# Kernel optimization log

Hardware: AMD Instinct MI355X
Metric: run time of the kernel (lower is better)

Reference implementation:

```python
import jax, jax.numpy as jnp
import numpy as np

E = 8          # num experts
TOPK = 2
D = 1024       # emb_size (expert hidden == emb_size)


def setup_inputs() -> dict:
    key = jax.random.key(0)
    ks = jax.random.split(key, 8)
    s = 1.0 / np.sqrt(D)
    x = jax.random.normal(ks[0], (4, 1024, D), dtype=jnp.float32)
    gate_W = jax.random.uniform(ks[1], (E, D), jnp.float32, -s, s)   # torch Linear weight (out,in)
    gate_b = jax.random.uniform(ks[2], (E,), jnp.float32, -s, s)
    w1 = jax.random.uniform(ks[3], (E, D, D), jnp.float32, -s, s)    # per-expert first Linear (out,in)
    b1 = jax.random.uniform(ks[4], (E, D), jnp.float32, -s, s)
    w2 = jax.random.uniform(ks[5], (E, D, D), jnp.float32, -s, s)    # per-expert second Linear (out,in)
    b2 = jax.random.uniform(ks[6], (E, D), jnp.float32, -s, s)
    return {"x": x, "gate_W": gate_W, "gate_b": gate_b,
            "w1": w1, "b1": b1, "w2": w2, "b2": b2}


def reference(x, gate_W, gate_b, w1, b1, w2, b2):
    x_shape = x.shape
    xt = x.reshape(-1, x_shape[-1])                       # [N, D]

    # gating
    gate_logits = xt @ gate_W.T + gate_b                  # [N, E]
    gate_prob = jax.nn.softmax(gate_logits, axis=-1)      # [N, E]
    top_w, top_i = jax.lax.top_k(gate_prob, TOPK)         # [N, K]
    top_w = jax.nn.softmax(top_w, axis=-1)                # renormalize over top-k

    # dense per-expert MLP: h = relu(x @ W1^T + b1); o = h @ W2^T + b2
    h = jax.nn.relu(jnp.einsum('nd,ehd->neh', xt, w1) + b1[None])   # [N, E, D]
    o = jnp.einsum('neh,eoh->neo', h, w2) + b2[None]                # [N, E, D]

    # gather top-k expert outputs per token and combine with weights
    o_top = jnp.take_along_axis(o, top_i[:, :, None], axis=1)       # [N, K, D]
    y = jnp.sum(o_top * top_w[:, :, None], axis=1)                  # [N, D]

    return y.reshape(x_shape), gate_prob
```

## Files before the change

kernel.cpp:

```cpp
#include <hip/hip_runtime.h>

#define NTOK 4096
#define DIM 1024
#define NE 8
#define NPAIR (NTOK * 2)

typedef __bf16 bf16x8 __attribute__((ext_vector_type(8)));
typedef float floatx4 __attribute__((ext_vector_type(4)));

__device__ __forceinline__ unsigned short f2bf(float f) {
  unsigned u = __float_as_uint(f);
  u = u + 0x7fffu + ((u >> 16) & 1u);
  return (unsigned short)(u >> 16);
}
__device__ __forceinline__ float bf2f(unsigned short h) {
  return __uint_as_float(((unsigned)h) << 16);
}

__device__ __forceinline__ void gld_lds16(const unsigned short* g, unsigned short* l) {
  __builtin_amdgcn_global_load_lds(
      (const __attribute__((address_space(1))) void*)g,
      (__attribute__((address_space(3))) void*)l, 16, 0, 0);
}

__global__ __launch_bounds__(256) void gate_kernel(
    const float* __restrict__ x, const float* __restrict__ gW,
    const float* __restrict__ gb,
    float* __restrict__ gp_out, int2* __restrict__ tops,
    float* __restrict__ pairw, int* __restrict__ cnt, int* __restrict__ done)
{
  const int tid = threadIdx.x;
  if (blockIdx.x == 0) {
    if (tid < NE) cnt[tid] = 0;
    if (tid == NE) *done = 0;
  }
  const int lane = tid & 63;
  const int wid = tid >> 6;
  const int t = blockIdx.x * 4 + wid;

  float4 xv[4];
#pragma unroll
  for (int j = 0; j < 4; j++)
    xv[j] = ((const float4*)(x + (size_t)t * DIM))[lane + 64 * j];

  float p[NE];
#pragma unroll
  for (int e = 0; e < NE; e++) {
    const float4* gwe = (const float4*)(gW + e * DIM);
    float s = 0.f;
#pragma unroll
    for (int j = 0; j < 4; j++) {
      float4 g = gwe[lane + 64 * j];
      s += xv[j].x * g.x + xv[j].y * g.y + xv[j].z * g.z + xv[j].w * g.w;
    }
    p[e] = s;
  }
#pragma unroll
  for (int e = 0; e < NE; e++) {
#pragma unroll
    for (int off = 32; off >= 1; off >>= 1) p[e] += __shfl_xor(p[e], off);
  }

  float m = -1e30f;
#pragma unroll
  for (int e = 0; e < NE; e++) { p[e] += gb[e]; m = fmaxf(m, p[e]); }
  float s = 0.f;
  float pr[NE];
#pragma unroll
  for (int e = 0; e < NE; e++) { pr[e] = __expf(p[e] - m); s += pr[e]; }
  float inv = 1.f / s;
#pragma unroll
  for (int e = 0; e < NE; e++) pr[e] *= inv;

  if (lane < NE) gp_out[(size_t)t * NE + lane] = pr[lane];

  if (lane == 0) {
    int i0 = 0;
#pragma unroll
    for (int e = 1; e < NE; e++) if (pr[e] > pr[i0]) i0 = e;
    int i1 = (i0 == 0) ? 1 : 0;
#pragma unroll
    for (int e = 0; e < NE; e++) if (e != i0 && pr[e] > pr[i1]) i1 = e;
    float d = __expf(pr[i1] - pr[i0]);
    float w0 = 1.f / (1.f + d);
    tops[t] = make_int2(i0, i1);
    pairw[t * 2] = w0;
    pairw[t * 2 + 1] = 1.f - w0;
  }
}

__global__ __launch_bounds__(256) void bin_sched_kernel(
    const int2* __restrict__ tops, int* __restrict__ cnt,
    int* __restrict__ bucket,
    int* __restrict__ posmap,
    int* __restrict__ done, int* __restrict__ base,
    int* __restrict__ sched, int* __restrict__ sched_n)
{
  const int t = blockIdx.x * 256 + threadIdx.x;
  const int lane = threadIdx.x & 63;
  int2 ti = tops[t];
#pragma unroll
  for (int slot = 0; slot < 2; slot++) {
    int e = slot ? ti.y : ti.x;
#pragma unroll
    for (int ex = 0; ex < NE; ex++) {
      bool mine = (e == ex);
      unsigned long long mask = __ballot(mine);
      if (mask) {
        int leader = __ffsll((long long)mask) - 1;
        int total = __popcll(mask);
        int prefix = __popcll(mask & ((1ull << lane) - 1ull));
        int idx = 0;
        if (lane == leader) idx = atomicAdd(&cnt[ex], total);
        idx = __shfl(idx, leader) + prefix;
        if (mine) {
          bucket[ex * NTOK + idx] = t * 2 + slot;
          posmap[t * 2 + slot] = (ex << 16) | idx;
        }
      }
    }
  }
  __syncthreads();
  if (threadIdx.x == 0) {
    if (atomicAdd(done, 1) == gridDim.x - 1) {
      int b = 0, pos = 0;
      for (int e = 0; e < NE; e++) {
        int c = atomicAdd(&cnt[e], 0);
        base[e] = b;
        int tiles = (c + 127) >> 7;
        for (int i = 0; i < tiles; i++) {
          int valid = c - i * 128; if (valid > 128) valid = 128;
          sched[pos++] = (e << 20) | (i << 8) | valid;
        }
        b += c;
      }
      base[NE] = b;
      *sched_n = pos;
    }
  }
}

__global__ __launch_bounds__(256) void cvt_kernel(
    const float4* __restrict__ src, ushort4* __restrict__ dst)
{
  const int i = blockIdx.x * 256 + threadIdx.x;
  float4 v = src[i];
  ushort4 o;
  o.x = f2bf(v.x); o.y = f2bf(v.y); o.z = f2bf(v.z); o.w = f2bf(v.w);
  dst[i] = o;
}

__global__ __launch_bounds__(256) void gather_kernel(
    const float* __restrict__ x, const int* __restrict__ bucket,
    const int* __restrict__ base, unsigned short* __restrict__ A_pack)
{
  const int p = blockIdx.x;
  int e = 0;
#pragma unroll
  for (int k = 0; k < NE - 1; k++) if (p >= base[k + 1]) e = k + 1;
  const int pair = bucket[e * NTOK + (p - base[e])];
  const int tok = pair >> 1;
  const int tid = threadIdx.x;
  float4 v = ((const float4*)(x + (size_t)tok * DIM))[tid];
  ushort4 o;
  o.x = f2bf(v.x); o.y = f2bf(v.y); o.z = f2bf(v.z); o.w = f2bf(v.w);
  ((ushort4*)(A_pack + (size_t)p * DIM))[tid] = o;
}

template <int RELU>
__global__ __launch_bounds__(256) void ffn_gemm(
    const unsigned short* __restrict__ A,
    const unsigned short* __restrict__ B,
    const float* __restrict__ bias,
    const int* __restrict__ base,
    const int* __restrict__ sched, const int* __restrict__ sched_n,
    unsigned short* __restrict__ Out)
{
  const int l = blockIdx.x;
  const int xcd = l & 7;
  const int w = l >> 3;
  const int nt = w & 7;
  const int slot = xcd * 9 + (w >> 3);
  if (slot >= *sched_n) return;
  const int se = sched[slot];
  const int e = se >> 20;
  const int mt = (se >> 8) & 0xfff;
  const int valid = se & 255;
  const int arow0 = base[e] + mt * 128;

  __shared__ unsigned short lda[128 * 64];
  __shared__ unsigned short ldb[128 * 64];

  const int tid = threadIdx.x;
  const int lane = tid & 63;
  const int wid = tid >> 6;

  const unsigned short* ap[4];
  const unsigned short* bp[4];
#pragma unroll
  for (int j = 0; j < 4; j++) {
    int g = wid * 4 + j;
    int row = g * 8 + (lane >> 3);
    int gran = (lane & 7) ^ (row & 7);
    int prow = arow0 + row;
    if (prow > NPAIR - 1) prow = NPAIR - 1;
    ap[j] = A + (size_t)prow * DIM + (gran << 3);
    bp[j] = B + ((size_t)e * DIM + nt * 128 + row) * DIM + (gran << 3);
  }

  floatx4 acc[4][4] = {};
  const int wm = (wid & 1) * 64;
  const int wn = (wid >> 1) * 64;
  const int quad = lane >> 4;
  const int cl = lane & 15;
  const int sw = cl & 7;

  for (int k0 = 0; k0 < 16; k0++) {
#pragma unroll
    for (int j = 0; j < 4; j++) {
      int g = wid * 4 + j;
      gld_lds16(ap[j], &lda[g * 512]);
      gld_lds16(bp[j], &ldb[g * 512]);
      ap[j] += 64;
      bp[j] += 64;
    }
    __syncthreads();
#pragma unroll
    for (int kk = 0; kk < 64; kk += 32) {
      const int gb = (kk >> 3) + quad;
      const int goff = ((gb ^ sw) << 3);
      bf16x8 af[4], bfr[4];
#pragma unroll
      for (int mi = 0; mi < 4; mi++)
        af[mi] = *(const bf16x8*)&lda[(wm + mi * 16 + cl) * 64 + goff];
#pragma unroll
      for (int ni = 0; ni < 4; ni++)
        bfr[ni] = *(const bf16x8*)&ldb[(wn + ni * 16 + cl) * 64 + goff];
#pragma unroll
      for (int mi = 0; mi < 4; mi++)
#pragma unroll
        for (int ni = 0; ni < 4; ni++)
          acc[mi][ni] = __builtin_amdgcn_mfma_f32_16x16x32_bf16(af[mi], bfr[ni], acc[mi][ni], 0, 0, 0);
    }
    if (k0 < 15) __syncthreads();
  }

#pragma unroll
  for (int ni = 0; ni < 4; ni++) {
    int col = nt * 128 + wn + ni * 16 + cl;
    float bval = bias[e * DIM + col];
#pragma unroll
    for (int mi = 0; mi < 4; mi++) {
#pragma unroll
      for (int reg = 0; reg < 4; reg++) {
        int rl = wm + mi * 16 + quad * 4 + reg;
        if (rl < valid) {
          float v = acc[mi][ni][reg] + bval;
          if (RELU) v = fmaxf(v, 0.f);
          Out[(size_t)(arow0 + rl) * DIM + col] = f2bf(v);
        }
      }
    }
  }
}

__global__ __launch_bounds__(256) void combine_kernel(
    const unsigned short* __restrict__ o, const int* __restrict__ posmap,
    const int* __restrict__ base, const float* __restrict__ pairw,
    float* __restrict__ y)
{
  const int t = blockIdx.x;
  const int tid = threadIdx.x;
  const int pm0 = posmap[t * 2], pm1 = posmap[t * 2 + 1];
  const int p0 = base[pm0 >> 16] + (pm0 & 0xffff);
  const int p1 = base[pm1 >> 16] + (pm1 & 0xffff);
  const float w0 = pairw[t * 2], w1 = pairw[t * 2 + 1];
  ushort4 a = ((const ushort4*)(o + (size_t)p0 * DIM))[tid];
  ushort4 b = ((const ushort4*)(o + (size_t)p1 * DIM))[tid];
  float4 r;
  r.x = w0 * bf2f(a.x) + w1 * bf2f(b.x);
  r.y = w0 * bf2f(a.y) + w1 * bf2f(b.y);
  r.z = w0 * bf2f(a.z) + w1 * bf2f(b.z);
  r.w = w0 * bf2f(a.w) + w1 * bf2f(b.w);
  ((float4*)(y + (size_t)t * DIM))[tid] = r;
}

extern "C" void kernel_launch(void* const* d_in, const int* in_sizes, int n_in,
                              void* d_out, int out_size, void* d_ws, size_t ws_size,
                              hipStream_t stream) {
  const float* x  = (const float*)d_in[0];
  const float* gW = (const float*)d_in[1];
  const float* gb = (const float*)d_in[2];
  const float* w1 = (const float*)d_in[3];
  const float* b1 = (const float*)d_in[4];
  const float* w2 = (const float*)d_in[5];
  const float* b2 = (const float*)d_in[6];
  float* y  = (float*)d_out;
  float* gp = (float*)d_out + (size_t)NTOK * DIM;

  char* ws = (char*)d_ws;
  unsigned short* A_pack = (unsigned short*)(ws);
  unsigned short* w2_bf  = (unsigned short*)(ws);
  unsigned short* h_pack = (unsigned short*)(ws + (size_t)(16u << 20));
  unsigned short* w1_bf  = (unsigned short*)(ws + (size_t)(32u << 20));
  unsigned short* o_pack = (unsigned short*)(ws + (size_t)(32u << 20));
  char* tail = ws + (size_t)(48u << 20);
  int*   cnt     = (int*)(tail);
  int*   done    = cnt + NE;
  int*   base    = done + 1;
  int*   sched   = base + NE + 1;
  int*   sched_n = sched + 128;
  int*   bucket  = sched_n + 1;
  float* pairw   = (float*)(bucket + NE * NTOK);
  int2*  tops    = (int2*)(pairw + NPAIR);
  int*   posmap  = (int*)(tops + NTOK);

  const int cvt_blocks = (NE * DIM * DIM / 4) / 256;
  gate_kernel<<<NTOK / 4, 256, 0, stream>>>(x, gW, gb, gp, tops, pairw, cnt, done);
  bin_sched_kernel<<<NTOK / 256, 256, 0, stream>>>(tops, cnt, bucket, posmap, done,
                                                   base, sched, sched_n);
  cvt_kernel<<<cvt_blocks, 256, 0, stream>>>((const float4*)w1, (ushort4*)w1_bf);
  gather_kernel<<<NPAIR, 256, 0, stream>>>(x, bucket, base, A_pack);
  ffn_gemm<1><<<576, 256, 0, stream>>>(A_pack, w1_bf, b1, base, sched, sched_n, h_pack);
  cvt_kernel<<<cvt_blocks, 256, 0, stream>>>((const float4*)w2, (ushort4*)w2_bf);
  ffn_gemm<0><<<576, 256, 0, stream>>>(h_pack, w2_bf, b2, base, sched, sched_n, o_pack);
  combine_kernel<<<NTOK, 256, 0, stream>>>(o_pack, posmap, base, pairw, y);
}
```

Measured before the change: 238.7 us.

## Halve GEMM N-tile, fuse w1 conversion into gather, pre-convert x in gate

The expert GEMMs now use a 128x64 output tile instead of 128x128, with twice as many blocks (1152) and a new slot/tile mapping across XCDs, to raise occupancy and wave count. The w1 fp32->bf16 conversion is folded into the gather kernel (cvt_blocks equals NPAIR), removing one launch. The gate kernel also writes a bf16 copy of x, so the gather becomes a plain bf16 copy. Smaller tiles lower per-block reuse of A and add extra A loads in exchange for parallelism.

```diff
diff --git a/kernel.cpp b/kernel.cpp
--- a/kernel.cpp
+++ b/kernel.cpp
@@ -25,7 +25,7 @@
 
 __global__ __launch_bounds__(256) void gate_kernel(
     const float* __restrict__ x, const float* __restrict__ gW,
-    const float* __restrict__ gb,
+    const float* __restrict__ gb, unsigned short* __restrict__ x_bf,
     float* __restrict__ gp_out, int2* __restrict__ tops,
     float* __restrict__ pairw, int* __restrict__ cnt, int* __restrict__ done)
 {
@@ -42,6 +42,13 @@
 #pragma unroll
   for (int j = 0; j < 4; j++)
     xv[j] = ((const float4*)(x + (size_t)t * DIM))[lane + 64 * j];
+#pragma unroll
+  for (int j = 0; j < 4; j++) {
+    ushort4 xb;
+    xb.x = f2bf(xv[j].x); xb.y = f2bf(xv[j].y);
+    xb.z = f2bf(xv[j].z); xb.w = f2bf(xv[j].w);
+    ((ushort4*)(x_bf + (size_t)t * DIM))[lane + 64 * j] = xb;
+  }
 
   float p[NE];
 #pragma unroll
@@ -150,21 +157,29 @@
   dst[i] = o;
 }
 
-__global__ __launch_bounds__(256) void gather_kernel(
-    const float* __restrict__ x, const int* __restrict__ bucket,
-    const int* __restrict__ base, unsigned short* __restrict__ A_pack)
+__global__ __launch_bounds__(256) void gather_cvt_kernel(
+    const unsigned short* __restrict__ x_bf, const int* __restrict__ bucket,
+    const int* __restrict__ base, unsigned short* __restrict__ A_pack,
+    const float4* __restrict__ w1, ushort4* __restrict__ w1_bf)
 {
   const int p = blockIdx.x;
+  const int tid = threadIdx.x;
+
+  {
+    const int i = p * 256 + tid;
+    float4 v = w1[i];
+    ushort4 o;
+    o.x = f2bf(v.x); o.y = f2bf(v.y); o.z = f2bf(v.z); o.w = f2bf(v.w);
+    w1_bf[i] = o;
+  }
+
   int e = 0;
 #pragma unroll
   for (int k = 0; k < NE - 1; k++) if (p >= base[k + 1]) e = k + 1;
   const int pair = bucket[e * NTOK + (p - base[e])];
   const int tok = pair >> 1;
-  const int tid = threadIdx.x;
-  float4 v = ((const float4*)(x + (size_t)tok * DIM))[tid];
-  ushort4 o;
-  o.x = f2bf(v.x); o.y = f2bf(v.y); o.z = f2bf(v.z); o.w = f2bf(v.w);
-  ((ushort4*)(A_pack + (size_t)p * DIM))[tid] = o;
+  ((ushort4*)(A_pack + (size_t)p * DIM))[tid] =
+      ((const ushort4*)(x_bf + (size_t)tok * DIM))[tid];
 }
 
 template <int RELU>
@@ -178,9 +193,9 @@
 {
   const int l = blockIdx.x;
   const int xcd = l & 7;
-  const int w = l >> 3;
-  const int nt = w & 7;
-  const int slot = xcd * 9 + (w >> 3);
+  const int j = l >> 3;
+  const int nt = j & 15;
+  const int slot = (j >> 4) * 8 + xcd;
   if (slot >= *sched_n) return;
   const int se = sched[slot];
   const int e = se >> 20;
@@ -189,65 +204,71 @@
   const int arow0 = base[e] + mt * 128;
 
   __shared__ unsigned short lda[128 * 64];
-  __shared__ unsigned short ldb[128 * 64];
+  __shared__ unsigned short ldb[64 * 64];
 
   const int tid = threadIdx.x;
   const int lane = tid & 63;
   const int wid = tid >> 6;
 
   const unsigned short* ap[4];
-  const unsigned short* bp[4];
-#pragma unroll
-  for (int j = 0; j < 4; j++) {
-    int g = wid * 4 + j;
-    int row = g * 8 + (lane >> 3);
+  const unsigned short* bp[2];
+#pragma unroll
+  for (int j0 = 0; j0 < 4; j0++) {
+    int row = wid * 32 + j0 * 8 + (lane >> 3);
     int gran = (lane & 7) ^ (row & 7);
     int prow = arow0 + row;
     if (prow > NPAIR - 1) prow = NPAIR - 1;
-    ap[j] = A + (size_t)prow * DIM + (gran << 3);
-    bp[j] = B + ((size_t)e * DIM + nt * 128 + row) * DIM + (gran << 3);
-  }
-
-  floatx4 acc[4][4] = {};
+    ap[j0] = A + (size_t)prow * DIM + (gran << 3);
+  }
+#pragma unroll
+  for (int j0 = 0; j0 < 2; j0++) {
+    int brow = wid * 16 + j0 * 8 + (lane >> 3);
+    int gran = (lane & 7) ^ (brow & 7);
+    bp[j0] = B + ((size_t)e * DIM + nt * 64 + brow) * DIM + (gran << 3);
+  }
+
+  floatx4 acc[4][2] = {};
   const int wm = (wid & 1) * 64;
-  const int wn = (wid >> 1) * 64;
+  const int wn = (wid >> 1) * 32;
   const int quad = lane >> 4;
   const int cl = lane & 15;
   const int sw = cl & 7;
 
   for (int k0 = 0; k0 < 16; k0++) {
 #pragma unroll
-    for (int j = 0; j < 4; j++) {
-      int g = wid * 4 + j;
-      gld_lds16(ap[j], &lda[g * 512]);
-      gld_lds16(bp[j], &ldb[g * 512]);
-      ap[j] += 64;
-      bp[j] += 64;
+    for (int j0 = 0; j0 < 4; j0++) {
+      gld_lds16(ap[j0], &lda[(wid * 32 + j0 * 8) * 64]);
+      ap[j0] += 64;
+    }
+#pragma unroll
+    for (int j0 = 0; j0 < 2; j0++) {
+      gld_lds16(bp[j0], &ldb[(wid * 16 + j0 * 8) * 64]);
+      bp[j0] += 64;
     }
     __syncthreads();
 #pragma unroll
     for (int kk = 0; kk < 64; kk += 32) {
       const int gb = (kk >> 3) + quad;
       const int goff = ((gb ^ sw) << 3);
-      bf16x8 af[4], bfr[4];
+      bf16x8 af[4], bfr[2];
 #pragma unroll
       for (int mi = 0; mi < 4; mi++)
         af[mi] = *(const bf16x8*)&lda[(wm + mi * 16 + cl) * 64 + goff];
 #pragma unroll
-      for (int ni = 0; ni < 4; ni++)
+      for (int ni = 0; ni < 2; ni++)
         bfr[ni] = *(const bf16x8*)&ldb[(wn + ni * 16 + cl) * 64 + goff];
 #pragma unroll
       for (int mi = 0; mi < 4; mi++)
 #pragma unroll
-        for (int ni = 0; ni < 4; ni++)
+        for (int ni = 0; ni < 2; ni++)
           acc[mi][ni] = __builtin_amdgcn_mfma_f32_16x16x32_bf16(af[mi], bfr[ni], acc[mi][ni], 0, 0, 0);
     }
     if (k0 < 15) __syncthreads();
   }
 
 #pragma unroll
-  for (int ni = 0; ni < 4; ni++) {
-    int col = nt * 128 + wn + ni * 16 + cl;
+  for (int ni = 0; ni < 2; ni++) {
+    int col = nt * 64 + wn + ni * 16 + cl;
     float bval = bias[e * DIM + col];
 #pragma unroll
     for (int mi = 0; mi < 4; mi++) {
@@ -304,7 +325,8 @@
   unsigned short* h_pack = (unsigned short*)(ws + (size_t)(16u << 20));
   unsigned short* w1_bf  = (unsigned short*)(ws + (size_t)(32u << 20));
   unsigned short* o_pack = (unsigned short*)(ws + (size_t)(32u << 20));
-  char* tail = ws + (size_t)(48u << 20);
+  unsigned short* x_bf   = (unsigned short*)(ws + (size_t)(48u << 20));
+  char* tail = ws + (size_t)(56u << 20);
   int*   cnt     = (int*)(tail);
   int*   done    = cnt + NE;
   int*   base    = done + 1;
@@ -316,13 +338,13 @@
   int*   posmap  = (int*)(tops + NTOK);
 
   const int cvt_blocks = (NE * DIM * DIM / 4) / 256;
-  gate_kernel<<<NTOK / 4, 256, 0, stream>>>(x, gW, gb, gp, tops, pairw, cnt, done);
+  gate_kernel<<<NTOK / 4, 256, 0, stream>>>(x, gW, gb, x_bf, gp, tops, pairw, cnt, done);
   bin_sched_kernel<<<NTOK / 256, 256, 0, stream>>>(tops, cnt, bucket, posmap, done,
                                                    base, sched, sched_n);
-  cvt_kernel<<<cvt_blocks, 256, 0, stream>>>((const float4*)w1, (ushort4*)w1_bf);
-  gather_kernel<<<NPAIR, 256, 0, stream>>>(x, bucket, base, A_pack);
-  ffn_gemm<1><<<576, 256, 0, stream>>>(A_pack, w1_bf, b1, base, sched, sched_n, h_pack);
+  gather_cvt_kernel<<<NPAIR, 256, 0, stream>>>(x_bf, bucket, base, A_pack,
+                                               (const float4*)w1, (ushort4*)w1_bf);
+  ffn_gemm<1><<<1152, 256, 0, stream>>>(A_pack, w1_bf, b1, base, sched, sched_n, h_pack);
   cvt_kernel<<<cvt_blocks, 256, 0, stream>>>((const float4*)w2, (ushort4*)w2_bf);
-  ffn_gemm<0><<<576, 256, 0, stream>>>(h_pack, w2_bf, b2, base, sched, sched_n, o_pack);
+  ffn_gemm<0><<<1152, 256, 0, stream>>>(h_pack, w2_bf, b2, base, sched, sched_n, o_pack);
   combine_kernel<<<NTOK, 256, 0, stream>>>(o_pack, posmap, base, pairw, y);
 }
```

After: 246.0 us. 1.03x slower.

## Split-K both expert GEMMs, fuse combine via atomics, merge w1 cvt into gather

Applied to the files above, without the earlier changes.

Both expert GEMMs now split the K dimension in two, doubling the grid from 576 to 1152 blocks for better CU occupancy. The first GEMM writes two bf16 partials, and a new reduce kernel adds them with the bias and ReLU. The second GEMM atomically accumulates weighted outputs straight into y after a memset, which removes the combine kernel and posmap. The w1 conversion is folded into the gather kernel. The cost is an extra partial-sum pass, bf16 rounding of partials, float atomic contention, and a memset.

```diff
diff --git a/kernel.cpp b/kernel.cpp
--- a/kernel.cpp
+++ b/kernel.cpp
@@ -92,7 +92,6 @@
 __global__ __launch_bounds__(256) void bin_sched_kernel(
     const int2* __restrict__ tops, int* __restrict__ cnt,
     int* __restrict__ bucket,
-    int* __restrict__ posmap,
     int* __restrict__ done, int* __restrict__ base,
     int* __restrict__ sched, int* __restrict__ sched_n)
 {
@@ -113,10 +112,7 @@
         int idx = 0;
         if (lane == leader) idx = atomicAdd(&cnt[ex], total);
         idx = __shfl(idx, leader) + prefix;
-        if (mine) {
-          bucket[ex * NTOK + idx] = t * 2 + slot;
-          posmap[t * 2 + slot] = (ex << 16) | idx;
-        }
+        if (mine) bucket[ex * NTOK + idx] = t * 2 + slot;
       }
     }
   }
@@ -150,43 +146,58 @@
   dst[i] = o;
 }
 
-__global__ __launch_bounds__(256) void gather_kernel(
+__global__ __launch_bounds__(256) void gather_cvt_kernel(
     const float* __restrict__ x, const int* __restrict__ bucket,
-    const int* __restrict__ base, unsigned short* __restrict__ A_pack)
+    const int* __restrict__ base, unsigned short* __restrict__ A_pack,
+    const float4* __restrict__ w1, ushort4* __restrict__ w1_bf)
 {
   const int p = blockIdx.x;
+  const int tid = threadIdx.x;
+
+  {
+    const int i = p * 256 + tid;
+    float4 v = w1[i];
+    ushort4 o;
+    o.x = f2bf(v.x); o.y = f2bf(v.y); o.z = f2bf(v.z); o.w = f2bf(v.w);
+    w1_bf[i] = o;
+  }
+
   int e = 0;
 #pragma unroll
   for (int k = 0; k < NE - 1; k++) if (p >= base[k + 1]) e = k + 1;
   const int pair = bucket[e * NTOK + (p - base[e])];
   const int tok = pair >> 1;
-  const int tid = threadIdx.x;
   float4 v = ((const float4*)(x + (size_t)tok * DIM))[tid];
   ushort4 o;
   o.x = f2bf(v.x); o.y = f2bf(v.y); o.z = f2bf(v.z); o.w = f2bf(v.w);
   ((ushort4*)(A_pack + (size_t)p * DIM))[tid] = o;
 }
 
-template <int RELU>
+template <int MODE>
 __global__ __launch_bounds__(256) void ffn_gemm(
     const unsigned short* __restrict__ A,
     const unsigned short* __restrict__ B,
     const float* __restrict__ bias,
     const int* __restrict__ base,
     const int* __restrict__ sched, const int* __restrict__ sched_n,
-    unsigned short* __restrict__ Out)
+    const int* __restrict__ bucket, const float* __restrict__ pairw,
+    unsigned short* __restrict__ P_lo, unsigned short* __restrict__ P_hi,
+    float* __restrict__ y)
 {
   const int l = blockIdx.x;
   const int xcd = l & 7;
-  const int w = l >> 3;
-  const int nt = w & 7;
-  const int slot = xcd * 9 + (w >> 3);
+  const int j = l >> 3;
+  const int nt = j & 7;
+  const int unit = (j >> 3) * 8 + xcd;
+  const int slot = unit >> 1;
+  const int half = unit & 1;
   if (slot >= *sched_n) return;
   const int se = sched[slot];
   const int e = se >> 20;
   const int mt = (se >> 8) & 0xfff;
   const int valid = se & 255;
   const int arow0 = base[e] + mt * 128;
+  const int kbase = half * 512;
 
   __shared__ unsigned short lda[128 * 64];
   __shared__ unsigned short ldb[128 * 64];
@@ -198,14 +209,13 @@
   const unsigned short* ap[4];
   const unsigned short* bp[4];
 #pragma unroll
-  for (int j = 0; j < 4; j++) {
-    int g = wid * 4 + j;
-    int row = g * 8 + (lane >> 3);
+  for (int j0 = 0; j0 < 4; j0++) {
+    int row = wid * 32 + j0 * 8 + (lane >> 3);
     int gran = (lane & 7) ^ (row & 7);
     int prow = arow0 + row;
     if (prow > NPAIR - 1) prow = NPAIR - 1;
-    ap[j] = A + (size_t)prow * DIM + (gran << 3);
-    bp[j] = B + ((size_t)e * DIM + nt * 128 + row) * DIM + (gran << 3);
+    ap[j0] = A + (size_t)prow * DIM + kbase + (gran << 3);
+    bp[j0] = B + ((size_t)e * DIM + nt * 128 + row) * DIM + kbase + (gran << 3);
   }
 
   floatx4 acc[4][4] = {};
@@ -215,14 +225,14 @@
   const int cl = lane & 15;
   const int sw = cl & 7;
 
-  for (int k0 = 0; k0 < 16; k0++) {
-#pragma unroll
-    for (int j = 0; j < 4; j++) {
-      int g = wid * 4 + j;
-      gld_lds16(ap[j], &lda[g * 512]);
-      gld_lds16(bp[j], &ldb[g * 512]);
-      ap[j] += 64;
-      bp[j] += 64;
+  for (int k0 = 0; k0 < 8; k0++) {
+#pragma unroll
+    for (int j0 = 0; j0 < 4; j0++) {
+      int g = wid * 4 + j0;
+      gld_lds16(ap[j0], &lda[g * 512]);
+      gld_lds16(bp[j0], &ldb[g * 512]);
+      ap[j0] += 64;
+      bp[j0] += 64;
     }
     __syncthreads();
 #pragma unroll
@@ -242,47 +252,75 @@
         for (int ni = 0; ni < 4; ni++)
           acc[mi][ni] = __builtin_amdgcn_mfma_f32_16x16x32_bf16(af[mi], bfr[ni], acc[mi][ni], 0, 0, 0);
     }
-    if (k0 < 15) __syncthreads();
-  }
-
-#pragma unroll
-  for (int ni = 0; ni < 4; ni++) {
-    int col = nt * 128 + wn + ni * 16 + cl;
-    float bval = bias[e * DIM + col];
+    if (k0 < 7) __syncthreads();
+  }
+
+  if (MODE == 0) {
+    unsigned short* P = half ? P_hi : P_lo;
+#pragma unroll
+    for (int ni = 0; ni < 4; ni++) {
+      int col = nt * 128 + wn + ni * 16 + cl;
+#pragma unroll
+      for (int mi = 0; mi < 4; mi++) {
+#pragma unroll
+        for (int reg = 0; reg < 4; reg++) {
+          int rl = wm + mi * 16 + quad * 4 + reg;
+          if (rl < valid)
+            P[(size_t)(arow0 + rl) * DIM + col] = f2bf(acc[mi][ni][reg]);
+        }
+      }
+    }
+  } else {
+    float wrow[16];
+    int trow[16];
 #pragma unroll
     for (int mi = 0; mi < 4; mi++) {
 #pragma unroll
       for (int reg = 0; reg < 4; reg++) {
         int rl = wm + mi * 16 + quad * 4 + reg;
         if (rl < valid) {
-          float v = acc[mi][ni][reg] + bval;
-          if (RELU) v = fmaxf(v, 0.f);
-          Out[(size_t)(arow0 + rl) * DIM + col] = f2bf(v);
+          int pair = bucket[e * NTOK + mt * 128 + rl];
+          wrow[mi * 4 + reg] = pairw[pair];
+          trow[mi * 4 + reg] = pair >> 1;
         }
       }
     }
-  }
-}
-
-__global__ __launch_bounds__(256) void combine_kernel(
-    const unsigned short* __restrict__ o, const int* __restrict__ posmap,
-    const int* __restrict__ base, const float* __restrict__ pairw,
-    float* __restrict__ y)
-{
-  const int t = blockIdx.x;
-  const int tid = threadIdx.x;
-  const int pm0 = posmap[t * 2], pm1 = posmap[t * 2 + 1];
-  const int p0 = base[pm0 >> 16] + (pm0 & 0xffff);
-  const int p1 = base[pm1 >> 16] + (pm1 & 0xffff);
-  const float w0 = pairw[t * 2], w1 = pairw[t * 2 + 1];
-  ushort4 a = ((const ushort4*)(o + (size_t)p0 * DIM))[tid];
-  ushort4 b = ((const ushort4*)(o + (size_t)p1 * DIM))[tid];
-  float4 r;
-  r.x = w0 * bf2f(a.x) + w1 * bf2f(b.x);
-  r.y = w0 * bf2f(a.y) + w1 * bf2f(b.y);
-  r.z = w0 * bf2f(a.z) + w1 * bf2f(b.z);
-  r.w = w0 * bf2f(a.w) + w1 * bf2f(b.w);
-  ((float4*)(y + (size_t)t * DIM))[tid] = r;
+#pragma unroll
+    for (int ni = 0; ni < 4; ni++) {
+      int col = nt * 128 + wn + ni * 16 + cl;
+      float bh = 0.5f * bias[e * DIM + col];
+#pragma unroll
+      for (int mi = 0; mi < 4; mi++) {
+#pragma unroll
+        for (int reg = 0; reg < 4; reg++) {
+          int rl = wm + mi * 16 + quad * 4 + reg;
+          if (rl < valid)
+            atomicAdd(&y[(size_t)trow[mi * 4 + reg] * DIM + col],
+                      wrow[mi * 4 + reg] * (acc[mi][ni][reg] + bh));
+        }
+      }
+    }
+  }
+}
+
+__global__ __launch_bounds__(256) void reduce1_kernel(
+    unsigned short* __restrict__ P_lo, const unsigned short* __restrict__ P_hi,
+    const float* __restrict__ b1, const int* __restrict__ base)
+{
+  const int i = blockIdx.x * 256 + threadIdx.x;
+  const int p = i >> 8;
+  int e = 0;
+#pragma unroll
+  for (int k = 0; k < NE - 1; k++) if (p >= base[k + 1]) e = k + 1;
+  ushort4 a = ((const ushort4*)P_lo)[i];
+  ushort4 b = ((const ushort4*)P_hi)[i];
+  float4 bb = ((const float4*)(b1 + e * DIM))[i & 255];
+  ushort4 o;
+  o.x = f2bf(fmaxf(bf2f(a.x) + bf2f(b.x) + bb.x, 0.f));
+  o.y = f2bf(fmaxf(bf2f(a.y) + bf2f(b.y) + bb.y, 0.f));
+  o.z = f2bf(fmaxf(bf2f(a.z) + bf2f(b.z) + bb.z, 0.f));
+  o.w = f2bf(fmaxf(bf2f(a.w) + bf2f(b.w) + bb.w, 0.f));
+  ((ushort4*)P_lo)[i] = o;
 }
 
 extern "C" void kernel_launch(void* const* d_in, const int* in_sizes, int n_in,
@@ -301,9 +339,10 @@
   char* ws = (char*)d_ws;
   unsigned short* A_pack = (unsigned short*)(ws);
   unsigned short* w2_bf  = (unsigned short*)(ws);
-  unsigned short* h_pack = (unsigned short*)(ws + (size_t)(16u << 20));
-  unsigned short* w1_bf  = (unsigned short*)(ws + (size_t)(32u << 20));
-  unsigned short* o_pack = (unsigned short*)(ws + (size_t)(32u << 20));
+  unsigned short* w1_bf  = (unsigned short*)(ws + (size_t)(16u << 20));
+  unsigned short* P_lo   = (unsigned short*)(ws + (size_t)(32u << 20));
+  unsigned short* h_pack = P_lo;
+  unsigned short* P_hi   = (unsigned short*)y;
   char* tail = ws + (size_t)(48u << 20);
   int*   cnt     = (int*)(tail);
   int*   done    = cnt + NE;
@@ -313,16 +352,18 @@
   int*   bucket  = sched_n + 1;
   float* pairw   = (float*)(bucket + NE * NTOK);
   int2*  tops    = (int2*)(pairw + NPAIR);
-  int*   posmap  = (int*)(tops + NTOK);
-
-  const int cvt_blocks = (NE * DIM * DIM / 4) / 256;
+
   gate_kernel<<<NTOK / 4, 256, 0, stream>>>(x, gW, gb, gp, tops, pairw, cnt, done);
-  bin_sched_kernel<<<NTOK / 256, 256, 0, stream>>>(tops, cnt, bucket, posmap, done,
+  bin_sched_kernel<<<NTOK / 256, 256, 0, stream>>>(tops, cnt, bucket, done,
                                                    base, sched, sched_n);
-  cvt_kernel<<<cvt_blocks, 256, 0, stream>>>((const float4*)w1, (ushort4*)w1_bf);
-  gather_kernel<<<NPAIR, 256, 0, stream>>>(x, bucket, base, A_pack);
-  ffn_gemm<1><<<576, 256, 0, stream>>>(A_pack, w1_bf, b1, base, sched, sched_n, h_pack);
-  cvt_kernel<<<cvt_blocks, 256, 0, stream>>>((const float4*)w2, (ushort4*)w2_bf);
-  ffn_gemm<0><<<576, 256, 0, stream>>>(h_pack, w2_bf, b2, base, sched, sched_n, o_pack);
-  combine_kernel<<<NTOK, 256, 0, stream>>>(o_pack, posmap, base, pairw, y);
-}
+  gather_cvt_kernel<<<NPAIR, 256, 0, stream>>>(x, bucket, base, A_pack,
+                                               (const float4*)w1, (ushort4*)w1_bf);
+  ffn_gemm<0><<<1152, 256, 0, stream>>>(A_pack, w1_bf, b1, base, sched, sched_n,
+                                        bucket, pairw, P_lo, P_hi, y);
+  reduce1_kernel<<<NPAIR * DIM / 1024, 256, 0, stream>>>(P_lo, P_hi, b1, base);
+  cvt_kernel<<<(NE * DIM * DIM / 4) / 256, 256, 0, stream>>>(
+      (const float4*)w2, (ushort4*)w2_bf);
+  hipMemsetAsync(y, 0, (size_t)NTOK * DIM * sizeof(float), stream);
+  ffn_gemm<1><<<1152, 256, 0, stream>>>(h_pack, w2_bf, b2, base, sched, sched_n,
+                                        bucket, pairw, nullptr, nullptr, y);
+}
```

Result: slower. 280.2 us (+17.4%).
